# Kernel optimization log

Hardware: AMD Instinct MI355X
Metric: run time of the kernel (lower is better)

## Reference

```python
import jax, jax.numpy as jnp
import numpy as np

CH = 512
GROUPS = 32
EPS = 1e-6


def setup_inputs() -> dict:
    key = jax.random.key(0)
    ks = jax.random.split(key, 12)
    b, c, h, w = 4, CH, 64, 64
    std = 1.0 / np.sqrt(c)
    return {
        "x": jax.random.normal(ks[0], (b, c, h, w), dtype=jnp.float32),
        "norm_gamma": jnp.ones((c,), jnp.float32),
        "norm_beta": jnp.zeros((c,), jnp.float32),
        "wq": jax.random.normal(ks[1], (c, c), jnp.float32) * std,
        "bq": jax.random.normal(ks[2], (c,), jnp.float32) * 0.01,
        "wk": jax.random.normal(ks[3], (c, c), jnp.float32) * std,
        "bk": jax.random.normal(ks[4], (c,), jnp.float32) * 0.01,
        "wv": jax.random.normal(ks[5], (c, c), jnp.float32) * std,
        "bv": jax.random.normal(ks[6], (c,), jnp.float32) * 0.01,
        "wo": jax.random.normal(ks[7], (c, c), jnp.float32) * std,
        "bo": jax.random.normal(ks[8], (c,), jnp.float32) * 0.01,
    }


def _group_norm(x, gamma, beta):
    b, c, h, w = x.shape
    xg = x.reshape(b, GROUPS, c // GROUPS, h, w)
    mean = xg.mean(axis=(2, 3, 4), keepdims=True)
    var = xg.var(axis=(2, 3, 4), keepdims=True)
    xn = ((xg - mean) * jax.lax.rsqrt(var + EPS)).reshape(b, c, h, w)
    return xn * gamma[None, :, None, None] + beta[None, :, None, None]


def reference(x, norm_gamma, norm_beta, wq, bq, wk, bk, wv, bv, wo, bo):
    b, c, h, w = x.shape
    hn = _group_norm(x, norm_gamma, norm_beta)
    hs = hn.reshape(b, c, h * w)  # [b, c, n]
    # 1x1 convs == per-pixel matmuls over channel dim (weight[out,in])
    q = jnp.einsum('oc,bcn->bno', wq, hs) + bq  # [b, n, c]
    k = jnp.einsum('oc,bcn->bon', wk, hs) + bk[None, :, None]  # [b, c, n]
    v = jnp.einsum('oc,bcn->bno', wv, hs) + bv  # [b, n, c]
    scale = c ** (-0.5)
    attn = jax.nn.softmax(jnp.einsum('bnc,bcm->bnm', q, k) * scale, axis=-1)
    out = jnp.einsum('bnm,bmc->bnc', attn, v)  # [b, n, c]
    out = jnp.einsum('oc,bnc->bon', wo, out) + bo[None, :, None]  # [b, c, n]
    return x + out.reshape(b, c, h, w)
```

## Files before the change

### kernel.cpp

```cpp
#include <hip/hip_runtime.h>
#include <hip/hip_bf16.h>
#include <cstdint>

typedef __bf16 bf16;
typedef __bf16 bf16x8 __attribute__((ext_vector_type(8)));
typedef __bf16 bf16x4 __attribute__((ext_vector_type(4)));
typedef float f32x4 __attribute__((ext_vector_type(4)));

__device__ __forceinline__ void gld_lds16(const void* g, void* l) {
  __builtin_amdgcn_global_load_lds((const __attribute__((address_space(1))) void*)g,
                                   (__attribute__((address_space(3))) void*)l, 16, 0, 0);
}

enum { BIAS_NONE = 0, BIAS_COL = 1, BIAS_ROW = 2, BIAS_QK = 3 };
enum { OUT_BF16 = 0, OUT_F32_RESID = 1 };

template<int BIAS_MODE, int OUT_MODE>
__global__ __launch_bounds__(256)
void gemm_bt(const bf16* __restrict__ A, long sA, int lda,
             const bf16* __restrict__ Bm, long sB, int ldb,
             void* __restrict__ Cv, long sC, int ldc,
             const float* __restrict__ bias, const float* __restrict__ bias2,
             const float* __restrict__ resid, long sR,
             int K, float scale)
{
  const int bm = blockIdx.x, bn = blockIdx.y, bz = blockIdx.z;
  const char* Ab = (const char*)(A + (long)bz * sA);
  const char* Bb = (const char*)(Bm + (long)bz * sB);
  const int tid = threadIdx.x;
  const int wave = tid >> 6, lane = tid & 63;
  const int wr = wave >> 1, wc = wave & 1;

  __shared__ __attribute__((aligned(128))) char lds[32768];
  char* ldsA = lds;
  char* ldsB = lds + 16384;

  uint32_t aoff[4], boff[4];
#pragma unroll
  for (int i = 0; i < 4; ++i) {
    uint32_t ra = (uint32_t)(wr * 64 + i * 16 + (lane & 15));
    uint32_t la = ra * 128u + (uint32_t)((lane >> 4) << 4);
    aoff[i] = la ^ ((la >> 3) & 0x70u);
    uint32_t rb = (uint32_t)(wc * 64 + i * 16 + (lane & 15));
    uint32_t lb = rb * 128u + (uint32_t)((lane >> 4) << 4);
    boff[i] = lb ^ ((lb >> 3) & 0x70u);
  }
  uint32_t srow[4], sinb[4];
#pragma unroll
  for (int t = 0; t < 4; ++t) {
    uint32_t paddr = (uint32_t)(((wave * 4 + t) * 64 + lane) * 16);
    uint32_t laddr = paddr ^ ((paddr >> 3) & 0x70u);
    srow[t] = laddr >> 7;
    sinb[t] = laddr & 127u;
  }

  const long ldab = (long)lda * 2, ldbb = (long)ldb * 2;
  const long arow0 = (long)bm * 128, brow0 = (long)bn * 128;
  f32x4 acc[4][4] = {};
  const int nK = K >> 6;
  for (int kt = 0; kt < nK; ++kt) {
    const long k0b = (long)kt * 128;
#pragma unroll
    for (int t = 0; t < 4; ++t) {
      gld_lds16(Ab + (arow0 + srow[t]) * ldab + k0b + sinb[t], ldsA + (wave * 4 + t) * 1024);
      gld_lds16(Bb + (brow0 + srow[t]) * ldbb + k0b + sinb[t], ldsB + (wave * 4 + t) * 1024);
    }
    __syncthreads();
#pragma unroll
    for (int kk = 0; kk < 2; ++kk) {
      bf16x8 af[4], bfr[4];
#pragma unroll
      for (int i = 0; i < 4; ++i) {
        af[i]  = *(const bf16x8*)(ldsA + (aoff[i] ^ (kk << 6)));
        bfr[i] = *(const bf16x8*)(ldsB + (boff[i] ^ (kk << 6)));
      }
#pragma unroll
      for (int mi = 0; mi < 4; ++mi)
#pragma unroll
        for (int ni = 0; ni < 4; ++ni)
          acc[mi][ni] = __builtin_amdgcn_mfma_f32_16x16x32_bf16(af[mi], bfr[ni], acc[mi][ni], 0, 0, 0);
    }
    __syncthreads();
  }

  const int cl = lane & 15, rq = lane >> 4;
  const long row0 = (long)bm * 128 + wr * 64;
  const long col0 = (long)bn * 128 + wc * 64;

  if constexpr (OUT_MODE == OUT_F32_RESID) {
    float* Co = (float*)Cv + (long)bz * sC;
    const float* X = resid + (long)bz * sR;
#pragma unroll
    for (int mi = 0; mi < 4; ++mi)
#pragma unroll
      for (int ni = 0; ni < 4; ++ni) {
        const long col = col0 + ni * 16 + cl;
#pragma unroll
        for (int j = 0; j < 4; ++j) {
          const long row = row0 + mi * 16 + rq * 4 + j;
          Co[row * ldc + col] = acc[mi][ni][j] + bias[row] + X[row * ldc + col];
        }
      }
  } else if constexpr (BIAS_MODE == BIAS_QK) {
    const bool isq = (col0 < 512);
    bf16* base = (bf16*)Cv + (long)bz * sC + (isq ? 0 : sR);
    const long csub = isq ? 0 : 512;
#pragma unroll
    for (int mi = 0; mi < 4; ++mi)
#pragma unroll
      for (int ni = 0; ni < 4; ++ni) {
        const long col = col0 + ni * 16 + cl;
        const float bc = isq ? bias[col] * scale : bias2[col - 512];
        const float vs = isq ? scale : 1.f;
#pragma unroll
        for (int j = 0; j < 4; ++j) {
          const long row = row0 + mi * 16 + rq * 4 + j;
          base[row * ldc + (col - csub)] = (bf16)(acc[mi][ni][j] * vs + bc);
        }
      }
  } else {
    bf16* Co = (bf16*)Cv + (long)bz * sC;
#pragma unroll
    for (int mi = 0; mi < 4; ++mi)
#pragma unroll
      for (int ni = 0; ni < 4; ++ni) {
        const long col = col0 + ni * 16 + cl;
        float bc = 0.f;
        if (BIAS_MODE == BIAS_COL) bc = bias[col] * scale;
#pragma unroll
        for (int j = 0; j < 4; ++j) {
          const long row = row0 + mi * 16 + rq * 4 + j;
          float v = acc[mi][ni][j] * (BIAS_MODE == BIAS_COL ? scale : 1.f) + bc;
          if (BIAS_MODE == BIAS_ROW) v += bias[row];
          Co[row * ldc + col] = (bf16)v;
        }
      }
  }
}

__global__ __launch_bounds__(256)
void sm_scan(const bf16* __restrict__ S, float2* __restrict__ rs)
{
  const long row = (long)blockIdx.x * 4 + (threadIdx.x >> 6);
  const int lane = threadIdx.x & 63;
  const bf16* p = S + row * 4096;
  float v[64];
#pragma unroll
  for (int i = 0; i < 8; ++i) {
    bf16x8 c = *(const bf16x8*)(p + (i * 64 + lane) * 8);
#pragma unroll
    for (int j = 0; j < 8; ++j) v[i * 8 + j] = (float)c[j];
  }
  float m = -3.0e38f;
#pragma unroll
  for (int i = 0; i < 64; ++i) m = fmaxf(m, v[i]);
#pragma unroll
  for (int d = 32; d > 0; d >>= 1) m = fmaxf(m, __shfl_xor(m, d, 64));
  float s = 0.f;
#pragma unroll
  for (int i = 0; i < 64; ++i) s += __expf(v[i] - m);
#pragma unroll
  for (int d = 32; d > 0; d >>= 1) s += __shfl_xor(s, d, 64);
  if (lane == 0) rs[row] = make_float2(m, 1.f / s);
}

__global__ __launch_bounds__(512, 1)
void gemm_pv3(const bf16* __restrict__ S, long sA,
              const bf16* __restrict__ Vm, long sB,
              bf16* __restrict__ O, long sC,
              const float2* __restrict__ rstat, long sRS, int swz)
{
  constexpr int T = 64;
  extern __shared__ char lds[];
  char* ldsA = lds;
  char* ldsB = lds + 16384;

  int bm, bz;
  if (swz) {
    const int bid = blockIdx.x;
    const int xcd = bid & 7;
    bz = xcd >> 1;
    bm = ((bid >> 3) << 1) | (xcd & 1);
  } else {
    bm = blockIdx.x; bz = blockIdx.z;
  }
  const char* Ab = (const char*)(S + (long)bz * sA) + (long)bm * 64 * 8192;
  const char* Bb = (const char*)(Vm + (long)bz * sB);
  const float2* rs = rstat + (long)bz * sRS;
  const int tid = threadIdx.x, wave = tid >> 6, lane = tid & 63;
  const int lg = lane >> 4, l15 = lane & 15;

  const uint32_t ar = (uint32_t)(tid >> 3), ab0 = (uint32_t)((tid & 7) * 16);
  const float Mr = rs[bm * 64 + ar].x;

  uint32_t bR[8], bIn[8];
#pragma unroll
  for (int j = 0; j < 8; ++j) {
    uint32_t s = (uint32_t)(j * 512 + tid);
    bR[j] = s >> 3;
    bIn[j] = (s & 7) * 16;
  }

  uint32_t aO[4], bO[4];
#pragma unroll
  for (int mi = 0; mi < 4; ++mi) {
    uint32_t r = (uint32_t)(mi * 16 + l15);
    aO[mi] = r * 128 + (((uint32_t)(lg * 16)) ^ ((r & 7) << 4));
  }
#pragma unroll
  for (int ni = 0; ni < 4; ++ni) {
    uint32_t r = (uint32_t)(wave * 64 + ni * 16 + l15);
    bO[ni] = r * 128 + (((uint32_t)(lg * 16)) ^ ((r & 7) << 4));
  }

  f32x4 acc[4][4] = {};

  auto stageB = [&](uint32_t nb, int t) {
#pragma unroll
    for (int j = 0; j < 8; ++j)
      gld_lds16(Bb + (long)bR[j] * 8192 + (long)t * 128 + (bIn[j] ^ ((bR[j] & 7) << 4)),
                ldsB + nb * 65536 + bR[j] * 128 + bIn[j]);
  };
  auto loadA = [&](int t) -> bf16x8 {
    return *(const bf16x8*)(Ab + (long)ar * 8192 + (long)t * 128 + ab0);
  };
  auto writeA = [&](uint32_t nb, bf16x8 sv) {
    bf16x8 pv;
#pragma unroll
    for (int j = 0; j < 8; ++j)
      pv[j] = (bf16)__expf((float)sv[j] - Mr);
    *(bf16x8*)(ldsA + nb * 8192 + ar * 128 + (ab0 ^ ((ar & 7) << 4))) = pv;
  };

  {
    bf16x8 sv0 = loadA(0);
    stageB(0, 0);
    writeA(0, sv0);
  }
  bf16x8 svn = loadA(1);
  stageB(1, 1);
  asm volatile("s_waitcnt vmcnt(9)" ::: "memory");
  asm volatile("s_waitcnt lgkmcnt(0)" ::: "memory");
  __builtin_amdgcn_sched_barrier(0);
  __builtin_amdgcn_s_barrier();

  for (int t = 0; t < T; ++t) {
    const uint32_t cur = (uint32_t)(t & 1), nxt = cur ^ 1u;

    bf16x8 af[4][2], bfr[4][2];
#pragma unroll
    for (int mi = 0; mi < 4; ++mi)
#pragma unroll
      for (int kk = 0; kk < 2; ++kk)
        af[mi][kk] = *(const bf16x8*)(ldsA + ((cur * 8192 + aO[mi]) ^ (uint32_t)(kk << 6)));
#pragma unroll
    for (int ni = 0; ni < 4; ++ni)
#pragma unroll
      for (int kk = 0; kk < 2; ++kk)
        bfr[ni][kk] = *(const bf16x8*)(ldsB + ((cur * 65536 + bO[ni]) ^ (uint32_t)(kk << 6)));

    if (t + 1 < T) writeA(nxt, svn);

    asm volatile("s_waitcnt lgkmcnt(0)" ::: "memory");
    __builtin_amdgcn_sched_barrier(0);
    __builtin_amdgcn_s_barrier();

    if (t + 2 < T) {
      svn = loadA(t + 2);
      stageB(cur, t + 2);
    }

    __builtin_amdgcn_s_setprio(1);
#pragma unroll
    for (int mi = 0; mi < 4; ++mi)
#pragma unroll
      for (int ni = 0; ni < 4; ++ni)
#pragma unroll
        for (int kk = 0; kk < 2; ++kk)
          acc[mi][ni] = __builtin_amdgcn_mfma_f32_16x16x32_bf16(af[mi][kk], bfr[ni][kk], acc[mi][ni], 0, 0, 0);
    __builtin_amdgcn_s_setprio(0);

    if (t + 1 < T) {
      if (t + 2 < T) asm volatile("s_waitcnt vmcnt(9)" ::: "memory");
      else           asm volatile("s_waitcnt vmcnt(0)" ::: "memory");
      __builtin_amdgcn_s_barrier();
    }
  }

  bf16* Co = O + (long)bz * sC + (long)bm * 64 * 512;
#pragma unroll
  for (int mi = 0; mi < 4; ++mi)
#pragma unroll
    for (int j = 0; j < 4; ++j) {
      const int row = mi * 16 + lg * 4 + j;
      const float invL = rs[bm * 64 + row].y;
#pragma unroll
      for (int ni = 0; ni < 4; ++ni) {
        const int col = wave * 64 + ni * 16 + l15;
        Co[(long)row * 512 + col] = (bf16)(acc[mi][ni][j] * invL);
      }
    }
}

__global__ __launch_bounds__(256)
void gn_stats(const float* __restrict__ x, float* __restrict__ stats)
{
  const int bg = blockIdx.x;
  const float4* px = (const float4*)(x + (long)bg * 65536);
  float s1 = 0.f, s2 = 0.f;
  for (int i = threadIdx.x; i < 16384; i += 256) {
    float4 f = px[i];
    s1 += f.x + f.y + f.z + f.w;
    s2 += f.x * f.x + f.y * f.y + f.z * f.z + f.w * f.w;
  }
#pragma unroll
  for (int d = 32; d > 0; d >>= 1) {
    s1 += __shfl_xor(s1, d, 64);
    s2 += __shfl_xor(s2, d, 64);
  }
  __shared__ float r1[4], r2[4];
  const int wave = threadIdx.x >> 6, lane = threadIdx.x & 63;
  if (lane == 0) { r1[wave] = s1; r2[wave] = s2; }
  __syncthreads();
  if (threadIdx.x == 0) {
    float t1 = r1[0] + r1[1] + r1[2] + r1[3];
    float t2 = r2[0] + r2[1] + r2[2] + r2[3];
    float mean = t1 * (1.f / 65536.f);
    float var  = t2 * (1.f / 65536.f) - mean * mean;
    stats[bg * 2]     = mean;
    stats[bg * 2 + 1] = rsqrtf(var + 1e-6f);
  }
}

__global__ __launch_bounds__(256)
void gn_apply(const float* __restrict__ x, const float* __restrict__ stats,
              const float* __restrict__ gamma, const float* __restrict__ beta,
              bf16* __restrict__ hn)
{
  const int b = blockIdx.y;
  const int n0 = blockIdx.x * 64;
  __shared__ __attribute__((aligned(16))) char lt[65536];
  const int tid = threadIdx.x;
  for (int i = 0; i < 32; ++i) {
    int f = i * 256 + tid;
    int c = f >> 4;
    int n4 = f & 15;
    float4 xv = *(const float4*)(x + (((long)b * 512 + c) * 4096) + n0 + n4 * 4);
    int g = c >> 4;
    float mean = stats[(b * 32 + g) * 2];
    float rstd = stats[(b * 32 + g) * 2 + 1];
    float ga = gamma[c], be = beta[c];
    float y[4];
    y[0] = (xv.x - mean) * rstd * ga + be;
    y[1] = (xv.y - mean) * rstd * ga + be;
    y[2] = (xv.z - mean) * rstd * ga + be;
    y[3] = (xv.w - mean) * rstd * ga + be;
    uint32_t cb = (uint32_t)(c * 2);
#pragma unroll
    for (int jj = 0; jj < 4; ++jj) {
      uint32_t nl = (uint32_t)(n4 * 4 + jj);
      uint32_t phys = nl * 1024u + (cb ^ (((nl >> 2) & 7u) << 4));
      *(bf16*)(lt + phys) = (bf16)y[jj];
    }
  }
  __syncthreads();
  for (int i = 0; i < 16; ++i) {
    int j = i * 256 + tid;
    uint32_t row = (uint32_t)(j >> 6);
    uint32_t m = (uint32_t)(j & 63);
    uint32_t phys = row * 1024u + ((m * 16u) ^ (((row >> 2) & 7u) << 4));
    uint4 val = *(const uint4*)(lt + phys);
    *(uint4*)((char*)(hn + ((long)b * 4096 + n0 + row) * 512) + m * 16) = val;
  }
}

__global__ __launch_bounds__(256)
void conv_w4(const float* __restrict__ w0, const float* __restrict__ w1,
             const float* __restrict__ w2, const float* __restrict__ w3,
             bf16* __restrict__ dst)
{
  const int z = blockIdx.y;
  const float* src = (z == 0) ? w0 : (z == 1) ? w1 : (z == 2) ? w2 : w3;
  const int i = blockIdx.x * 256 + threadIdx.x;
  float4 f = ((const float4*)src)[i];
  bf16x4 o;
  o[0] = (bf16)f.x; o[1] = (bf16)f.y; o[2] = (bf16)f.z; o[3] = (bf16)f.w;
  ((bf16x4*)(dst))[(long)z * 65536 + i] = o;
}

extern "C" void kernel_launch(void* const* d_in, const int* in_sizes, int n_in,
                              void* d_out, int out_size, void* d_ws, size_t ws_size,
                              hipStream_t stream)
{
  const float* x     = (const float*)d_in[0];
  const float* gamma = (const float*)d_in[1];
  const float* beta  = (const float*)d_in[2];
  const float* wq = (const float*)d_in[3];
  const float* bq = (const float*)d_in[4];
  const float* wk = (const float*)d_in[5];
  const float* bk = (const float*)d_in[6];
  const float* wv = (const float*)d_in[7];
  const float* bv = (const float*)d_in[8];
  const float* wo = (const float*)d_in[9];
  const float* bo = (const float*)d_in[10];
  float* out = (float*)d_out;

  char* ws = (char*)d_ws;
  bf16* hn  = (bf16*)(ws + 0);
  bf16* q   = (bf16*)(ws + 16777216);
  bf16* k   = (bf16*)(ws + 33554432);
  bf16* v   = (bf16*)(ws + 50331648);
  bf16* O   = (bf16*)(ws + 67108864);
  bf16* wqb = (bf16*)(ws + 83886080);
  bf16* wvb = (bf16*)(ws + 84934656);
  bf16* wob = (bf16*)(ws + 85458944);
  float* gstats = (float*)(ws + 85983232);
  float2* rstat = (float2*)(ws + 85984256);
  bf16* S   = (bf16*)(ws + 86115328);

  const long sBC = 2097152;
  const long sS1 = 16777216;
  const long K_OFS = 8388608;
  const float scale = 0.044194173824159216f;

  const int LDS_PV = 147456;
  hipFuncSetAttribute(reinterpret_cast<const void*>(gemm_pv3),
                      hipFuncAttributeMaxDynamicSharedMemorySize, LDS_PV);

  conv_w4<<<dim3(256, 4), 256, 0, stream>>>(wq, wk, wv, wo, wqb);
  gn_stats<<<128, 256, 0, stream>>>(x, gstats);
  gn_apply<<<dim3(64, 4), 256, 0, stream>>>(x, gstats, gamma, beta, hn);

  gemm_bt<BIAS_QK, OUT_BF16><<<dim3(32, 8, 4), 256, 0, stream>>>(
      hn, sBC, 512, wqb, 0, 512, q, sBC, 512,
      bq, bk, nullptr, K_OFS, 512, scale);
  gemm_bt<BIAS_ROW, OUT_BF16><<<dim3(4, 32, 4), 256, 0, stream>>>(
      wvb, 0, 512, hn, sBC, 512, v, sBC, 4096,
      bv, nullptr, nullptr, 0, 512, 1.f);

  const bool tier1 = ws_size >= (size_t)220333056;
  if (tier1) {
    gemm_bt<BIAS_NONE, OUT_BF16><<<dim3(32, 32, 4), 256, 0, stream>>>(
        q, sBC, 512, k, sBC, 512, S, sS1, 4096,
        nullptr, nullptr, nullptr, 0, 512, 1.f);
    sm_scan<<<4096, 256, 0, stream>>>(S, (float2*)rstat);
    gemm_pv3<<<dim3(256, 1, 1), 512, LDS_PV, stream>>>(
        S, sS1, v, sBC, O, sBC, rstat, 4096, 1);
  } else {
    for (int b = 0; b < 4; ++b) {
      gemm_bt<BIAS_NONE, OUT_BF16><<<dim3(32, 32, 1), 256, 0, stream>>>(
          q + b * sBC, 0, 512, k + b * sBC, 0, 512, S, 0, 4096,
          nullptr, nullptr, nullptr, 0, 512, 1.f);
      sm_scan<<<1024, 256, 0, stream>>>(S, (float2*)rstat);
      gemm_pv3<<<dim3(64, 1, 1), 512, LDS_PV, stream>>>(
          S, 0, v + b * sBC, 0, O + b * sBC, 0, rstat, 0, 0);
    }
  }

  gemm_bt<BIAS_ROW, OUT_F32_RESID><<<dim3(4, 32, 4), 256, 0, stream>>>(
      wob, 0, 512, O, sBC, 512, out, sBC, 4096,
      bo, nullptr, x, sBC, 512, 1.f);
}
```

Baseline: 299.3 us.

## Split PV GEMM into 64x256 tiles with 256-thread blocks for two-block occupancy

The P·V kernel now computes each 64-row output strip as two 256-column halves. Each half runs in its own 256-thread block, so the grid doubles and two blocks can share a CU. LDS per block drops from 147 KB to 80 KB, which allows that occupancy and more overlap across blocks. The cost is that each half re-reads the S tile and recomputes the exp() on it, doubling that work and its global traffic.

```diff
diff --git a/kernel.cpp b/kernel.cpp
--- a/kernel.cpp
+++ b/kernel.cpp
@@ -164,8 +164,8 @@
   if (lane == 0) rs[row] = make_float2(m, 1.f / s);
 }
 
-__global__ __launch_bounds__(512, 1)
-void gemm_pv3(const bf16* __restrict__ S, long sA,
+__global__ __launch_bounds__(256, 2)
+void gemm_pv4(const bf16* __restrict__ S, long sA,
               const bf16* __restrict__ Vm, long sB,
               bf16* __restrict__ O, long sC,
               const float2* __restrict__ rstat, long sRS, int swz)
@@ -175,31 +175,27 @@
   char* ldsA = lds;
   char* ldsB = lds + 16384;
 
-  int bm, bz;
+  int bm, bn, bz;
   if (swz) {
     const int bid = blockIdx.x;
     const int xcd = bid & 7;
     bz = xcd >> 1;
-    bm = ((bid >> 3) << 1) | (xcd & 1);
-  } else {
-    bm = blockIdx.x; bz = blockIdx.z;
-  }
+    bn = (bid >> 3) & 1;
+    bm = ((bid >> 4) << 1) | (xcd & 1);
+  } else { bm = blockIdx.x; bn = blockIdx.y; bz = blockIdx.z; }
+
   const char* Ab = (const char*)(S + (long)bz * sA) + (long)bm * 64 * 8192;
-  const char* Bb = (const char*)(Vm + (long)bz * sB);
+  const char* Bb = (const char*)(Vm + (long)bz * sB) + (long)bn * 256 * 8192;
   const float2* rs = rstat + (long)bz * sRS;
   const int tid = threadIdx.x, wave = tid >> 6, lane = tid & 63;
   const int lg = lane >> 4, l15 = lane & 15;
 
-  const uint32_t ar = (uint32_t)(tid >> 3), ab0 = (uint32_t)((tid & 7) * 16);
-  const float Mr = rs[bm * 64 + ar].x;
-
-  uint32_t bR[8], bIn[8];
-#pragma unroll
-  for (int j = 0; j < 8; ++j) {
-    uint32_t s = (uint32_t)(j * 512 + tid);
-    bR[j] = s >> 3;
-    bIn[j] = (s & 7) * 16;
-  }
+  const uint32_t ar0 = (uint32_t)(tid >> 3), ac16 = (uint32_t)((tid & 7) * 16);
+  const float Mr0 = rs[bm * 64 + ar0].x;
+  const float Mr1 = rs[bm * 64 + 32 + ar0].x;
+  const uint32_t aswz = (ar0 & 7) << 4;
+
+  const uint32_t bdst0 = (uint32_t)tid * 16;
 
   uint32_t aO[4], bO[4];
 #pragma unroll
@@ -217,29 +213,37 @@
 
   auto stageB = [&](uint32_t nb, int t) {
 #pragma unroll
-    for (int j = 0; j < 8; ++j)
-      gld_lds16(Bb + (long)bR[j] * 8192 + (long)t * 128 + (bIn[j] ^ ((bR[j] & 7) << 4)),
-                ldsB + nb * 65536 + bR[j] * 128 + bIn[j]);
+    for (int j = 0; j < 8; ++j) {
+      uint32_t row = (uint32_t)(j * 32) + ar0;
+      gld_lds16(Bb + (long)row * 8192 + (long)t * 128 + (ac16 ^ ((row & 7) << 4)),
+                ldsB + nb * 32768 + (uint32_t)(j * 4096) + bdst0);
+    }
   };
-  auto loadA = [&](int t) -> bf16x8 {
-    return *(const bf16x8*)(Ab + (long)ar * 8192 + (long)t * 128 + ab0);
+  auto loadA0 = [&](int t) -> bf16x8 {
+    return *(const bf16x8*)(Ab + (long)ar0 * 8192 + (long)t * 128 + ac16);
   };
-  auto writeA = [&](uint32_t nb, bf16x8 sv) {
-    bf16x8 pv;
-#pragma unroll
-    for (int j = 0; j < 8; ++j)
-      pv[j] = (bf16)__expf((float)sv[j] - Mr);
-    *(bf16x8*)(ldsA + nb * 8192 + ar * 128 + (ab0 ^ ((ar & 7) << 4))) = pv;
+  auto loadA1 = [&](int t) -> bf16x8 {
+    return *(const bf16x8*)(Ab + (long)(32 + ar0) * 8192 + (long)t * 128 + ac16);
   };
+  auto writeA = [&](uint32_t nb, bf16x8 s0, bf16x8 s1) {
+    bf16x8 p0, p1;
+#pragma unroll
+    for (int j = 0; j < 8; ++j) {
+      p0[j] = (bf16)__expf((float)s0[j] - Mr0);
+      p1[j] = (bf16)__expf((float)s1[j] - Mr1);
+    }
+    *(bf16x8*)(ldsA + nb * 8192 + ar0 * 128 + (ac16 ^ aswz)) = p0;
+    *(bf16x8*)(ldsA + nb * 8192 + (32 + ar0) * 128 + (ac16 ^ aswz)) = p1;
+  };
 
   {
-    bf16x8 sv0 = loadA(0);
+    bf16x8 s0 = loadA0(0), s1 = loadA1(0);
     stageB(0, 0);
-    writeA(0, sv0);
-  }
-  bf16x8 svn = loadA(1);
+    writeA(0, s0, s1);
+  }
+  bf16x8 an0 = loadA0(1), an1 = loadA1(1);
   stageB(1, 1);
-  asm volatile("s_waitcnt vmcnt(9)" ::: "memory");
+  asm volatile("s_waitcnt vmcnt(10)" ::: "memory");
   asm volatile("s_waitcnt lgkmcnt(0)" ::: "memory");
   __builtin_amdgcn_sched_barrier(0);
   __builtin_amdgcn_s_barrier();
@@ -257,16 +261,17 @@
     for (int ni = 0; ni < 4; ++ni)
 #pragma unroll
       for (int kk = 0; kk < 2; ++kk)
-        bfr[ni][kk] = *(const bf16x8*)(ldsB + ((cur * 65536 + bO[ni]) ^ (uint32_t)(kk << 6)));
-
-    if (t + 1 < T) writeA(nxt, svn);
+        bfr[ni][kk] = *(const bf16x8*)(ldsB + ((cur * 32768 + bO[ni]) ^ (uint32_t)(kk << 6)));
+
+    if (t + 1 < T) writeA(nxt, an0, an1);
 
     asm volatile("s_waitcnt lgkmcnt(0)" ::: "memory");
     __builtin_amdgcn_sched_barrier(0);
     __builtin_amdgcn_s_barrier();
 
     if (t + 2 < T) {
-      svn = loadA(t + 2);
+      an0 = loadA0(t + 2);
+      an1 = loadA1(t + 2);
       stageB(cur, t + 2);
     }
 
@@ -281,13 +286,13 @@
     __builtin_amdgcn_s_setprio(0);
 
     if (t + 1 < T) {
-      if (t + 2 < T) asm volatile("s_waitcnt vmcnt(9)" ::: "memory");
+      if (t + 2 < T) asm volatile("s_waitcnt vmcnt(10)" ::: "memory");
       else           asm volatile("s_waitcnt vmcnt(0)" ::: "memory");
       __builtin_amdgcn_s_barrier();
     }
   }
 
-  bf16* Co = O + (long)bz * sC + (long)bm * 64 * 512;
+  bf16* Co = O + (long)bz * sC + (long)bm * 64 * 512 + (long)bn * 256;
 #pragma unroll
   for (int mi = 0; mi < 4; ++mi)
 #pragma unroll
@@ -423,8 +428,8 @@
   const long K_OFS = 8388608;
   const float scale = 0.044194173824159216f;
 
-  const int LDS_PV = 147456;
-  hipFuncSetAttribute(reinterpret_cast<const void*>(gemm_pv3),
+  const int LDS_PV = 81920;
+  hipFuncSetAttribute(reinterpret_cast<const void*>(gemm_pv4),
                       hipFuncAttributeMaxDynamicSharedMemorySize, LDS_PV);
 
   conv_w4<<<dim3(256, 4), 256, 0, stream>>>(wq, wk, wv, wo, wqb);
@@ -444,7 +449,7 @@
         q, sBC, 512, k, sBC, 512, S, sS1, 4096,
         nullptr, nullptr, nullptr, 0, 512, 1.f);
     sm_scan<<<4096, 256, 0, stream>>>(S, (float2*)rstat);
-    gemm_pv3<<<dim3(256, 1, 1), 512, LDS_PV, stream>>>(
+    gemm_pv4<<<dim3(512, 1, 1), 256, LDS_PV, stream>>>(
         S, sS1, v, sBC, O, sBC, rstat, 4096, 1);
   } else {
     for (int b = 0; b < 4; ++b) {
@@ -452,7 +457,7 @@
           q + b * sBC, 0, 512, k + b * sBC, 0, 512, S, 0, 4096,
           nullptr, nullptr, nullptr, 0, 512, 1.f);
       sm_scan<<<1024, 256, 0, stream>>>(S, (float2*)rstat);
-      gemm_pv3<<<dim3(64, 1, 1), 512, LDS_PV, stream>>>(
+      gemm_pv4<<<dim3(64, 2, 1), 256, LDS_PV, stream>>>(
           S, 0, v + b * sBC, 0, O + b * sBC, 0, rstat, 0, 0);
     }
   }
```

Result: faster. 291.0 us (-2.8%).
